# Kernel optimization log

Measured on AMD Instinct MI355X. Metric: run time of the kernel, lower is better.

Reference implementation:

```python
import jax, jax.numpy as jnp
import numpy as np

S, B, D, DV = 2048, 16, 128, 128


def setup_inputs() -> dict:
    key = jax.random.key(0)
    kq, kk, kv = jax.random.split(key, 3)
    return {
        "query": jax.random.normal(kq, (S, B, D), dtype=jnp.float32),
        "key": jax.random.normal(kk, (S, B, D), dtype=jnp.float32),
        "value": jax.random.normal(kv, (S, B, DV), dtype=jnp.float32),
    }


def reference(query, key, value):
    # sim: [B, S_q, S_k]
    d = key.shape[-1]
    sim = jnp.einsum('sbd,tbd->bst', query, key) / jnp.sqrt(jnp.asarray(d, query.dtype))
    # causal mask: disallow attending to future positions (strictly upper triangle)
    sq, sk = sim.shape[-2], sim.shape[-1]
    causal = jnp.tril(jnp.ones((sq, sk), dtype=bool))  # [S_q, S_k]
    sim = jnp.where(causal[None, :, :], sim, -jnp.inf)
    a = jax.nn.softmax(sim, axis=-1)  # dropout omitted (eval mode, p=0)
    # context: [S_q, B, D_v]
    context = jnp.einsum('bst,tbe->sbe', a, value)
    return context
```

## Files before the change

kernel.cpp:

```cpp
#include <hip/hip_runtime.h>
#include <stdint.h>

#define SS 2048
#define BB 16
#define DD 128
#define DVV 128
#define BQ 32
#define BK 32
#define NTILES (SS / BK)
#define TILE_HW 4096

typedef __attribute__((ext_vector_type(8))) short short8;
typedef __attribute__((ext_vector_type(4))) float float4v;

typedef __attribute__((address_space(1))) const void glob_cv;
typedef __attribute__((address_space(3))) void lds_v;

__device__ __forceinline__ short f2bf(float f) {
  union { float f; uint32_t u; } x;
  x.f = f;
  uint32_t r = x.u + 0x7fffu + ((x.u >> 16) & 1u);
  return (short)(r >> 16);
}
__device__ __forceinline__ float bf2f(short h) {
  union { uint32_t u; float f; } y;
  y.u = ((uint32_t)(uint16_t)h) << 16;
  return y.f;
}

__device__ __forceinline__ int kappa(int quad, int j) {
  return (j < 4) ? (quad * 4 + j) : (16 + quad * 4 + (j - 4));
}

__global__ __launch_bounds__(256) void conv_kv(
    const float* __restrict__ kg, const float* __restrict__ vg,
    short* __restrict__ kimg, short* __restrict__ vimg) {
  __shared__ short tile[BK][136];
  const int t = blockIdx.x, b = blockIdx.y;
  if (blockIdx.z == 0) {
    short* out = kimg + ((size_t)(b * NTILES + t)) * TILE_HW;
#pragma unroll
    for (int p = 0; p < 2; ++p) {
      const int ch = threadIdx.x + p * 256;
      const int key = ch >> 4, c = ch & 15;
      const float* src = kg + ((size_t)(t * BK + key) * BB + b) * DD + c * 8;
      float4v f0 = *(const float4v*)src;
      float4v f1 = *(const float4v*)(src + 4);
      short8 s;
#pragma unroll
      for (int i = 0; i < 4; ++i) { s[i] = f2bf(f0[i]); s[4 + i] = f2bf(f1[i]); }
      *(short8*)(out + key * 128 + ((c ^ (key & 7)) * 8)) = s;
    }
  } else {
    short* out = vimg + ((size_t)(b * NTILES + t)) * TILE_HW;
#pragma unroll
    for (int p = 0; p < 2; ++p) {
      const int ch = threadIdx.x + p * 256;
      const int key = ch >> 4, fc = ch & 15;
      const float* src = vg + ((size_t)(t * BK + key) * BB + b) * DVV + fc * 8;
      float4v f0 = *(const float4v*)src;
      float4v f1 = *(const float4v*)(src + 4);
      short8 s;
#pragma unroll
      for (int i = 0; i < 4; ++i) { s[i] = f2bf(f0[i]); s[4 + i] = f2bf(f1[i]); }
      *(short8*)&tile[key][fc * 8] = s;
    }
    __syncthreads();
#pragma unroll
    for (int p = 0; p < 2; ++p) {
      const int idx = threadIdx.x + p * 256;
      const int nt = idx >> 6, quad = (idx >> 4) & 3, mm = idx & 15;
      const int dv = nt * 16 + mm;
      short8 s;
#pragma unroll
      for (int j = 0; j < 8; ++j) s[j] = tile[kappa(quad, j)][dv];
      *(short8*)(out + idx * 8) = s;
    }
  }
}

__global__ __launch_bounds__(256) void attn_fwd(
    const float* __restrict__ qg, const short* __restrict__ kimg,
    const short* __restrict__ vimg, float* __restrict__ og) {
  __shared__ __align__(16) short smem[8 * TILE_HW];

  const int tid  = threadIdx.x;
  const int tpar = tid >> 6;
  const int lane = tid & 63;
  const int m    = lane & 15;
  const int quad = lane >> 4;
  const int bid  = blockIdx.x;
  const int qt   = (NTILES - 1) - (bid >> 4);
  const int b    = bid & 15;
  const int q0   = qt * BQ;
  const int qrowA = q0 + m;
  const int qrowB = q0 + 16 + m;

  const float cscale = 0.08838834764831845f * 1.4426950408889634f;
  short8 qfragA[4], qfragB[4];
#pragma unroll
  for (int ks = 0; ks < 4; ++ks) {
    const float* qpA = qg + ((size_t)qrowA * BB + b) * DD + ks * 32 + quad * 8;
    const float* qpB = qg + ((size_t)qrowB * BB + b) * DD + ks * 32 + quad * 8;
    float4v a0 = *(const float4v*)qpA, a1 = *(const float4v*)(qpA + 4);
    float4v b0 = *(const float4v*)qpB, b1 = *(const float4v*)(qpB + 4);
    short8 fa, fb;
#pragma unroll
    for (int i = 0; i < 4; ++i) {
      fa[i] = f2bf(a0[i] * cscale); fa[4 + i] = f2bf(a1[i] * cscale);
      fb[i] = f2bf(b0[i] * cscale); fb[4 + i] = f2bf(b1[i] * cscale);
    }
    qfragA[ks] = fa; qfragB[ks] = fb;
  }

  float4v oaccA[8], oaccB[8];
#pragma unroll
  for (int i = 0; i < 8; ++i) {
    oaccA[i] = (float4v){0.f, 0.f, 0.f, 0.f};
    oaccB[i] = (float4v){0.f, 0.f, 0.f, 0.f};
  }
  float psumA = 0.f, psumB = 0.f;

  short* const kb = smem + tpar * TILE_HW;
  short* const vb = smem + (4 + tpar) * TILE_HW;
  const short* ksrc = kimg + (size_t)b * NTILES * TILE_HW + lane * 8;
  const short* vsrc = vimg + (size_t)b * NTILES * TILE_HW + lane * 8;

  const int ntile = qt + 1;
  for (int t = tpar; t < ntile; t += 4) {
    __builtin_amdgcn_s_waitcnt(0x0000);
    {
      const short* sk = ksrc + (size_t)t * TILE_HW;
      const short* sv2 = vsrc + (size_t)t * TILE_HW;
#pragma unroll
      for (int j = 0; j < 8; ++j) {
        __builtin_amdgcn_global_load_lds((glob_cv*)(sk + j * 512),
                                         (lds_v*)(kb + j * 512), 16, 0, 0);
        __builtin_amdgcn_global_load_lds((glob_cv*)(sv2 + j * 512),
                                         (lds_v*)(vb + j * 512), 16, 0, 0);
      }
    }
    __builtin_amdgcn_s_waitcnt(0x0F70);

    float4v sA0 = {0.f,0.f,0.f,0.f}, sA1 = {0.f,0.f,0.f,0.f};
    float4v sB0 = {0.f,0.f,0.f,0.f}, sB1 = {0.f,0.f,0.f,0.f};
#pragma unroll
    for (int ks = 0; ks < 4; ++ks) {
      const int c = ks * 4 + quad;
      short8 kf0 = *(const short8*)&kb[m * 128 + ((c ^ (m & 7)) * 8)];
      short8 kf1 = *(const short8*)&kb[(16 + m) * 128 + ((c ^ (m & 7)) * 8)];
      sA0 = __builtin_amdgcn_mfma_f32_16x16x32_bf16(kf0, qfragA[ks], sA0, 0, 0, 0);
      sA1 = __builtin_amdgcn_mfma_f32_16x16x32_bf16(kf1, qfragA[ks], sA1, 0, 0, 0);
      sB0 = __builtin_amdgcn_mfma_f32_16x16x32_bf16(kf0, qfragB[ks], sB0, 0, 0, 0);
      sB1 = __builtin_amdgcn_mfma_f32_16x16x32_bf16(kf1, qfragB[ks], sB1, 0, 0, 0);
    }
    float svA[8], svB[8];
#pragma unroll
    for (int r = 0; r < 4; ++r) {
      svA[r] = sA0[r]; svA[4 + r] = sA1[r];
      svB[r] = sB0[r]; svB[4 + r] = sB1[r];
    }

    const int kt0 = t * BK;
    if (kt0 + BK - 1 > q0) {
#pragma unroll
      for (int j = 0; j < 8; ++j)
        if (kt0 + kappa(quad, j) > qrowA) svA[j] = -1e30f;
    }
    if (kt0 + BK - 1 > q0 + 16) {
#pragma unroll
      for (int j = 0; j < 8; ++j)
        if (kt0 + kappa(quad, j) > qrowB) svB[j] = -1e30f;
    }

    short8 pfragA, pfragB;
#pragma unroll
    for (int j = 0; j < 8; ++j) {
      float pA = exp2f(svA[j]);
      float pB = exp2f(svB[j]);
      short hA = f2bf(pA), hB = f2bf(pB);
      pfragA[j] = hA; pfragB[j] = hB;
      psumA += bf2f(hA); psumB += bf2f(hB);
    }

#pragma unroll
    for (int nt = 0; nt < 8; ++nt) {
      short8 vf = *(const short8*)&vb[nt * 512 + lane * 8];
      oaccA[nt] = __builtin_amdgcn_mfma_f32_16x16x32_bf16(pfragA, vf, oaccA[nt], 0, 0, 0);
      oaccB[nt] = __builtin_amdgcn_mfma_f32_16x16x32_bf16(pfragB, vf, oaccB[nt], 0, 0, 0);
    }
  }

  __syncthreads();
  float* const cw = (float*)smem;
  if (tpar != 0) {
    float* p = cw + (size_t)((tpar - 1) * 64 + lane) * 67;
#pragma unroll
    for (int nt = 0; nt < 8; ++nt) {
      *(float4v*)(p + nt * 4)      = oaccA[nt];
      *(float4v*)(p + 32 + nt * 4) = oaccB[nt];
    }
    p[64] = psumA;
    p[65] = psumB;
  }
  __syncthreads();
  if (tpar == 0) {
#pragma unroll
    for (int w = 0; w < 3; ++w) {
      const float* p = cw + (size_t)(w * 64 + lane) * 67;
#pragma unroll
      for (int nt = 0; nt < 8; ++nt) {
        oaccA[nt] += *(const float4v*)(p + nt * 4);
        oaccB[nt] += *(const float4v*)(p + 32 + nt * 4);
      }
      psumA += p[64];
      psumB += p[65];
    }

    float lA = psumA, lB = psumB;
    lA += __shfl_xor(lA, 16, 64); lA += __shfl_xor(lA, 32, 64);
    lB += __shfl_xor(lB, 16, 64); lB += __shfl_xor(lB, 32, 64);
    const float liA = 1.0f / lA, liB = 1.0f / lB;
    float l4A[4], l4B[4];
#pragma unroll
    for (int rr = 0; rr < 4; ++rr) {
      l4A[rr] = __shfl(liA, quad * 4 + rr, 64);
      l4B[rr] = __shfl(liB, quad * 4 + rr, 64);
    }
#pragma unroll
    for (int rr = 0; rr < 4; ++rr) {
      const int gA = q0 + quad * 4 + rr;
      const int gB = q0 + 16 + quad * 4 + rr;
      float* opA = og + ((size_t)gA * BB + b) * DVV + m;
      float* opB = og + ((size_t)gB * BB + b) * DVV + m;
#pragma unroll
      for (int nt = 0; nt < 8; ++nt) {
        opA[nt * 16] = oaccA[nt][rr] * l4A[rr];
        opB[nt * 16] = oaccB[nt][rr] * l4B[rr];
      }
    }
  }
}

extern "C" void kernel_launch(void* const* d_in, const int* in_sizes, int n_in,
                              void* d_out, int out_size, void* d_ws, size_t ws_size,
                              hipStream_t stream) {
  const float* q = (const float*)d_in[0];
  const float* k = (const float*)d_in[1];
  const float* v = (const float*)d_in[2];
  float* out = (float*)d_out;
  short* kimg = (short*)d_ws;
  short* vimg = kimg + (size_t)BB * NTILES * TILE_HW;

  conv_kv<<<dim3(NTILES, BB, 2), 256, 0, stream>>>(k, v, kimg, vimg);
  attn_fwd<<<dim3(SS / BQ * BB), 256, 0, stream>>>(q, kimg, vimg, out);
}
```

Measured before the change: 140.8 us.

## Use single-wave blocks reading K/V fragments directly from global memory

Replaces the 4-wave block, which split key tiles across waves and staged K/V through LDS with async global-to-LDS loads, with one wave per block that walks all key tiles itself and loads MFMA fragments straight from global memory. This removes the LDS staging, the cross-wave reduction through shared memory and the barriers. In exchange each query tile is processed serially by one wave, so per-block latency grows with the causal tile count. The code also relies on L2/cache for K/V reuse and loses the latency hiding that the async copies gave.

```diff
diff --git a/kernel.cpp b/kernel.cpp
--- a/kernel.cpp
+++ b/kernel.cpp
@@ -13,9 +13,6 @@
 typedef __attribute__((ext_vector_type(8))) short short8;
 typedef __attribute__((ext_vector_type(4))) float float4v;
 
-typedef __attribute__((address_space(1))) const void glob_cv;
-typedef __attribute__((address_space(3))) void lds_v;
-
 __device__ __forceinline__ short f2bf(float f) {
   union { float f; uint32_t u; } x;
   x.f = f;
@@ -79,14 +76,10 @@
   }
 }
 
-__global__ __launch_bounds__(256) void attn_fwd(
+__global__ __launch_bounds__(64, 4) void attn_fwd(
     const float* __restrict__ qg, const short* __restrict__ kimg,
     const short* __restrict__ vimg, float* __restrict__ og) {
-  __shared__ __align__(16) short smem[8 * TILE_HW];
-
-  const int tid  = threadIdx.x;
-  const int tpar = tid >> 6;
-  const int lane = tid & 63;
+  const int lane = threadIdx.x & 63;
   const int m    = lane & 15;
   const int quad = lane >> 4;
   const int bid  = blockIdx.x;
@@ -121,34 +114,25 @@
   }
   float psumA = 0.f, psumB = 0.f;
 
-  short* const kb = smem + tpar * TILE_HW;
-  short* const vb = smem + (4 + tpar) * TILE_HW;
-  const short* ksrc = kimg + (size_t)b * NTILES * TILE_HW + lane * 8;
-  const short* vsrc = vimg + (size_t)b * NTILES * TILE_HW + lane * 8;
+  int koff[4][2];
+#pragma unroll
+  for (int ks = 0; ks < 4; ++ks) {
+    const int swz = ((ks * 4 + quad) ^ (m & 7)) * 8;
+    koff[ks][0] = m * 128 + swz;
+    koff[ks][1] = (16 + m) * 128 + swz;
+  }
+
+  const short* ktile = kimg + (size_t)(b * NTILES) * TILE_HW;
+  const short* vtile = vimg + (size_t)(b * NTILES) * TILE_HW;
 
   const int ntile = qt + 1;
-  for (int t = tpar; t < ntile; t += 4) {
-    __builtin_amdgcn_s_waitcnt(0x0000);
-    {
-      const short* sk = ksrc + (size_t)t * TILE_HW;
-      const short* sv2 = vsrc + (size_t)t * TILE_HW;
-#pragma unroll
-      for (int j = 0; j < 8; ++j) {
-        __builtin_amdgcn_global_load_lds((glob_cv*)(sk + j * 512),
-                                         (lds_v*)(kb + j * 512), 16, 0, 0);
-        __builtin_amdgcn_global_load_lds((glob_cv*)(sv2 + j * 512),
-                                         (lds_v*)(vb + j * 512), 16, 0, 0);
-      }
-    }
-    __builtin_amdgcn_s_waitcnt(0x0F70);
-
+  for (int t = 0; t < ntile; ++t, ktile += TILE_HW, vtile += TILE_HW) {
     float4v sA0 = {0.f,0.f,0.f,0.f}, sA1 = {0.f,0.f,0.f,0.f};
     float4v sB0 = {0.f,0.f,0.f,0.f}, sB1 = {0.f,0.f,0.f,0.f};
 #pragma unroll
     for (int ks = 0; ks < 4; ++ks) {
-      const int c = ks * 4 + quad;
-      short8 kf0 = *(const short8*)&kb[m * 128 + ((c ^ (m & 7)) * 8)];
-      short8 kf1 = *(const short8*)&kb[(16 + m) * 128 + ((c ^ (m & 7)) * 8)];
+      short8 kf0 = *(const short8*)(ktile + koff[ks][0]);
+      short8 kf1 = *(const short8*)(ktile + koff[ks][1]);
       sA0 = __builtin_amdgcn_mfma_f32_16x16x32_bf16(kf0, qfragA[ks], sA0, 0, 0, 0);
       sA1 = __builtin_amdgcn_mfma_f32_16x16x32_bf16(kf1, qfragA[ks], sA1, 0, 0, 0);
       sB0 = __builtin_amdgcn_mfma_f32_16x16x32_bf16(kf0, qfragB[ks], sB0, 0, 0, 0);
@@ -185,59 +169,32 @@
 
 #pragma unroll
     for (int nt = 0; nt < 8; ++nt) {
-      short8 vf = *(const short8*)&vb[nt * 512 + lane * 8];
+      short8 vf = *(const short8*)(vtile + nt * 512 + lane * 8);
       oaccA[nt] = __builtin_amdgcn_mfma_f32_16x16x32_bf16(pfragA, vf, oaccA[nt], 0, 0, 0);
       oaccB[nt] = __builtin_amdgcn_mfma_f32_16x16x32_bf16(pfragB, vf, oaccB[nt], 0, 0, 0);
     }
   }
 
-  __syncthreads();
-  float* const cw = (float*)smem;
-  if (tpar != 0) {
-    float* p = cw + (size_t)((tpar - 1) * 64 + lane) * 67;
+  float lA = psumA, lB = psumB;
+  lA += __shfl_xor(lA, 16, 64); lA += __shfl_xor(lA, 32, 64);
+  lB += __shfl_xor(lB, 16, 64); lB += __shfl_xor(lB, 32, 64);
+  const float liA = 1.0f / lA, liB = 1.0f / lB;
+  float l4A[4], l4B[4];
+#pragma unroll
+  for (int rr = 0; rr < 4; ++rr) {
+    l4A[rr] = __shfl(liA, quad * 4 + rr, 64);
+    l4B[rr] = __shfl(liB, quad * 4 + rr, 64);
+  }
+#pragma unroll
+  for (int rr = 0; rr < 4; ++rr) {
+    const int gA = q0 + quad * 4 + rr;
+    const int gB = q0 + 16 + quad * 4 + rr;
+    float* opA = og + ((size_t)gA * BB + b) * DVV + m;
+    float* opB = og + ((size_t)gB * BB + b) * DVV + m;
 #pragma unroll
     for (int nt = 0; nt < 8; ++nt) {
-      *(float4v*)(p + nt * 4)      = oaccA[nt];
-      *(float4v*)(p + 32 + nt * 4) = oaccB[nt];
-    }
-    p[64] = psumA;
-    p[65] = psumB;
-  }
-  __syncthreads();
-  if (tpar == 0) {
-#pragma unroll
-    for (int w = 0; w < 3; ++w) {
-      const float* p = cw + (size_t)(w * 64 + lane) * 67;
-#pragma unroll
-      for (int nt = 0; nt < 8; ++nt) {
-        oaccA[nt] += *(const float4v*)(p + nt * 4);
-        oaccB[nt] += *(const float4v*)(p + 32 + nt * 4);
-      }
-      psumA += p[64];
-      psumB += p[65];
-    }
-
-    float lA = psumA, lB = psumB;
-    lA += __shfl_xor(lA, 16, 64); lA += __shfl_xor(lA, 32, 64);
-    lB += __shfl_xor(lB, 16, 64); lB += __shfl_xor(lB, 32, 64);
-    const float liA = 1.0f / lA, liB = 1.0f / lB;
-    float l4A[4], l4B[4];
-#pragma unroll
-    for (int rr = 0; rr < 4; ++rr) {
-      l4A[rr] = __shfl(liA, quad * 4 + rr, 64);
-      l4B[rr] = __shfl(liB, quad * 4 + rr, 64);
-    }
-#pragma unroll
-    for (int rr = 0; rr < 4; ++rr) {
-      const int gA = q0 + quad * 4 + rr;
-      const int gB = q0 + 16 + quad * 4 + rr;
-      float* opA = og + ((size_t)gA * BB + b) * DVV + m;
-      float* opB = og + ((size_t)gB * BB + b) * DVV + m;
-#pragma unroll
-      for (int nt = 0; nt < 8; ++nt) {
-        opA[nt * 16] = oaccA[nt][rr] * l4A[rr];
-        opB[nt * 16] = oaccB[nt][rr] * l4B[rr];
-      }
+      opA[nt * 16] = oaccA[nt][rr] * l4A[rr];
+      opB[nt * 16] = oaccB[nt][rr] * l4B[rr];
     }
   }
 }
@@ -253,5 +210,5 @@
   short* vimg = kimg + (size_t)BB * NTILES * TILE_HW;
 
   conv_kv<<<dim3(NTILES, BB, 2), 256, 0, stream>>>(k, v, kimg, vimg);
-  attn_fwd<<<dim3(SS / BQ * BB), 256, 0, stream>>>(q, kimg, vimg, out);
-}
+  attn_fwd<<<dim3(SS / BQ * BB), 64, 0, stream>>>(q, kimg, vimg, out);
+}
```

Result: slower. 242.8 us (+72.5%).
